# Optimization experiments

Measured on AMD Instinct MI355X. Metric: run time of the kernel, lower is better.

## Reference

```python
import jax, jax.numpy as jnp
import numpy as np

D = 1024   # dim_embedding
H = 16     # n_head
HD = D // H


def setup_inputs() -> dict:
    key = jax.random.key(0)
    ks = jax.random.split(key, 5)
    B, T = 2, 2048
    x = jax.random.normal(ks[0], (B, T, D), dtype=jnp.float32)
    e = jax.random.normal(ks[1], (B, T, D), dtype=jnp.float32)
    s = 0.02
    W_en = jax.random.normal(ks[2], (D, 2 * D), dtype=jnp.float32) * s   # c_attn_en (k,v from encoder)
    W_q = jax.random.normal(ks[3], (D, D), dtype=jnp.float32) * s        # c_attn (q from decoder)
    W_o = jax.random.normal(ks[4], (D, D), dtype=jnp.float32) * s        # c_proj
    return {"x": x, "e": e, "W_en": W_en, "W_q": W_q, "W_o": W_o}


def reference(x, e, W_en, W_q, W_o):
    B, T, C = e.shape
    kv = e @ W_en                       # [B,T,2C]
    k, v = jnp.split(kv, 2, axis=-1)    # [B,T,C] each
    q = x @ W_q                         # [B,T,C]
    # reshape to heads: [B,H,T,hd]
    q = q.reshape(B, T, H, HD).transpose(0, 2, 1, 3)
    k = k.reshape(B, T, H, HD).transpose(0, 2, 1, 3)
    v = v.reshape(B, T, H, HD).transpose(0, 2, 1, 3)
    att = jnp.einsum("bhqd,bhkd->bhqk", q, k) * (1.0 / jnp.sqrt(jnp.float32(HD)))
    att = jax.nn.softmax(att, axis=-1)  # dropout=0 (eval)
    y = jnp.einsum("bhqk,bhkd->bhqd", att, v)
    y = y.transpose(0, 2, 1, 3).reshape(B, T, C)
    return y @ W_o
```

## Files before the change

kernel.cpp:

```cpp
#include <hip/hip_runtime.h>

typedef unsigned short u16;
typedef unsigned int u32;
typedef __bf16 bf16x8 __attribute__((ext_vector_type(8)));
typedef float f32x4 __attribute__((ext_vector_type(4)));

#define D_EMB 1024
#define T_SEQ 2048
#define NH 16
#define HD 64

#define GLB(p) ((const __attribute__((address_space(1))) unsigned int*)(p))
#define LDSP(p) ((__attribute__((address_space(3))) unsigned int*)(p))

__device__ __forceinline__ u16 f2bf(float f) {
  union { float f; unsigned u; } c; c.f = f;
  unsigned u = c.u;
  unsigned r = (u + 0x7FFFu + ((u >> 16) & 1u)) >> 16;
  return (u16)r;
}
__device__ __forceinline__ u32 fbits(float f) {
  union { float f; unsigned u; } c; c.f = f; return c.u;
}

__global__ __launch_bounds__(256) void cvt_kernel(const float* __restrict__ in,
                                                  u16* __restrict__ out, int n4) {
  int i = blockIdx.x * 256 + threadIdx.x;
  if (i < n4) {
    float4 v = reinterpret_cast<const float4*>(in)[i];
    ushort4 o;
    o.x = f2bf(v.x); o.y = f2bf(v.y); o.z = f2bf(v.z); o.w = f2bf(v.w);
    reinterpret_cast<ushort4*>(out)[i] = o;
  }
}

__global__ __launch_bounds__(256) void tconv_kernel(const float* __restrict__ in,
                                                    u16* __restrict__ out, int K, int N) {
  __shared__ float tile[32][33];
  int n0 = blockIdx.x * 32, k0 = blockIdx.y * 32;
  int tx = threadIdx.x, ty = threadIdx.y;
#pragma unroll
  for (int s = 0; s < 4; s++)
    tile[ty + 8 * s][tx] = in[(size_t)(k0 + ty + 8 * s) * N + n0 + tx];
  __syncthreads();
#pragma unroll
  for (int s = 0; s < 4; s++)
    out[(size_t)(n0 + ty + 8 * s) * K + k0 + tx] = f2bf(tile[tx][ty + 8 * s]);
}

__global__ __launch_bounds__(256) void proj_kernel(
    const u16* __restrict__ xb, const u16* __restrict__ eb,
    const u16* __restrict__ Wqt, const u16* __restrict__ Went,
    u16* __restrict__ qw, u16* __restrict__ kw, u16* __restrict__ vTw) {
  __shared__ u16 Al[128 * 64];
  __shared__ u16 Bl[128 * 64];
  const int tid = threadIdx.x;
  const int nb = blockIdx.x, mb = blockIdx.y;
  const int wave = tid >> 6, lane = tid & 63;
  const int ln15 = lane & 15, quad = lane >> 4;
  const int wm = wave & 1, wn = wave >> 1;

  const u16* A = (nb < 8) ? xb : eb;
  const u16* Wt = (nb < 8) ? (Wqt + (size_t)nb * 128 * D_EMB)
                           : (Went + ((size_t)nb * 128 - D_EMB) * D_EMB);

  const int grow = wave * 8 + (lane >> 3);
  const int g = (lane & 7) ^ ((lane >> 3) & 7);
  const u16* gA = A + (size_t)(mb * 128 + grow) * D_EMB + g * 8;
  const u16* gB = Wt + (size_t)grow * D_EMB + g * 8;
  char* lA = (char*)Al + wave * 1024;
  char* lB = (char*)Bl + wave * 1024;

  f32x4 acc[4][4] = {};

  for (int kb = 0; kb < D_EMB; kb += 64) {
#pragma unroll
    for (int it = 0; it < 4; it++) {
      __builtin_amdgcn_global_load_lds(GLB(gA + (size_t)it * 32 * D_EMB + kb), LDSP(lA + it * 4096), 16, 0, 0);
      __builtin_amdgcn_global_load_lds(GLB(gB + (size_t)it * 32 * D_EMB + kb), LDSP(lB + it * 4096), 16, 0, 0);
    }
    __syncthreads();
#pragma unroll
    for (int ks = 0; ks < 2; ks++) {
      bf16x8 af[4], bfr[4];
#pragma unroll
      for (int mt = 0; mt < 4; mt++) {
        int r = wm * 64 + mt * 16 + ln15;
        af[mt] = *reinterpret_cast<const bf16x8*>(&Al[r * 64 + (((ks * 4 + quad) ^ (r & 7)) * 8)]);
      }
#pragma unroll
      for (int nt = 0; nt < 4; nt++) {
        int r = wn * 64 + nt * 16 + ln15;
        bfr[nt] = *reinterpret_cast<const bf16x8*>(&Bl[r * 64 + (((ks * 4 + quad) ^ (r & 7)) * 8)]);
      }
#pragma unroll
      for (int mt = 0; mt < 4; mt++)
#pragma unroll
        for (int nt = 0; nt < 4; nt++)
          acc[mt][nt] = __builtin_amdgcn_mfma_f32_16x16x32_bf16(af[mt], bfr[nt], acc[mt][nt], 0, 0, 0);
    }
    __syncthreads();
  }

  const float QSCL = 0.125f * 1.44269504f;
#pragma unroll
  for (int mt = 0; mt < 4; mt++) {
#pragma unroll
    for (int nt = 0; nt < 4; nt++) {
#pragma unroll
      for (int i = 0; i < 4; i++) {
        int rr = mb * 128 + wm * 64 + mt * 16 + quad * 4 + i;
        int c  = nb * 128 + wn * 64 + nt * 16 + ln15;
        float v = acc[mt][nt][i];
        int b = rr >> 11, t = rr & 2047;
        if (c < D_EMB) {
          int h = c >> 6, d = c & 63;
          qw[(((size_t)(b * NH + h)) * T_SEQ + t) * HD + d] = f2bf(v * QSCL);
        } else if (c < 2 * D_EMB) {
          int cc = c - D_EMB; int h = cc >> 6, d = cc & 63;
          kw[(((size_t)(b * NH + h)) * T_SEQ + t) * HD + d] = f2bf(v);
        } else {
          int cc = c - 2 * D_EMB; int h = cc >> 6, d = cc & 63;
          vTw[(((size_t)(b * NH + h)) * HD + d) * T_SEQ + t] = f2bf(v);
        }
      }
    }
  }
}

__global__ __launch_bounds__(256) void attn_kernel(
    const u16* __restrict__ q, const u16* __restrict__ k,
    const u16* __restrict__ vT, u16* __restrict__ y) {
  __shared__ u16 Kl[64][64];
  __shared__ u16 Vl[64][64];
  __shared__ u16 Pl[4][16][72];

  const int bh = blockIdx.y;
  const int qt = blockIdx.x;
  const int tid = threadIdx.x;
  const int wave = tid >> 6, lane = tid & 63;
  const int ln15 = lane & 15, quad = lane >> 4;
  const int b = bh >> 4, h = bh & 15;

  const int qrow = qt * 64 + wave * 16 + ln15;
  const u16* qbase = q + ((size_t)bh * T_SEQ + qrow) * HD;
  bf16x8 qf[2];
  qf[0] = *reinterpret_cast<const bf16x8*>(qbase + quad * 8);
  qf[1] = *reinterpret_cast<const bf16x8*>(qbase + 32 + quad * 8);

  f32x4 o[4] = {};
  float lp = 0.f;

  const int srow = (lane >> 3) & 7;
  const int sch  = lane & 7;
  const int gch  = sch ^ srow;
  const u16* kg0 = k  + ((size_t)bh * T_SEQ + wave * 16 + srow) * HD + gch * 8;
  const u16* kg1 = kg0 + 8 * HD;
  const u16* vg0 = vT + ((size_t)bh * HD + wave * 16 + srow) * T_SEQ + gch * 8;
  const u16* vg1 = vg0 + 8 * T_SEQ;
  char* klb = (char*)&Kl[0][0] + wave * 2048;
  char* vlb = (char*)&Vl[0][0] + wave * 2048;

  for (int kt0 = 0; kt0 < T_SEQ; kt0 += 64) {
    __builtin_amdgcn_global_load_lds(GLB(kg0 + (size_t)kt0 * HD), LDSP(klb),        16, 0, 0);
    __builtin_amdgcn_global_load_lds(GLB(kg1 + (size_t)kt0 * HD), LDSP(klb + 1024), 16, 0, 0);
    __builtin_amdgcn_global_load_lds(GLB(vg0 + kt0),              LDSP(vlb),        16, 0, 0);
    __builtin_amdgcn_global_load_lds(GLB(vg1 + kt0),              LDSP(vlb + 1024), 16, 0, 0);
    __syncthreads();

    f32x4 s[4] = {};
#pragma unroll
    for (int ks = 0; ks < 2; ks++)
#pragma unroll
      for (int nt = 0; nt < 4; nt++) {
        int r = nt * 16 + ln15;
        bf16x8 kf = *reinterpret_cast<const bf16x8*>(&Kl[r][(((ks * 4 + quad) ^ (r & 7)) * 8)]);
        s[nt] = __builtin_amdgcn_mfma_f32_16x16x32_bf16(kf, qf[ks], s[nt], 0, 0, 0);
      }

#pragma unroll
    for (int nt = 0; nt < 4; nt++) {
      float p0 = __builtin_amdgcn_exp2f(s[nt][0]);
      float p1 = __builtin_amdgcn_exp2f(s[nt][1]);
      float p2 = __builtin_amdgcn_exp2f(s[nt][2]);
      float p3 = __builtin_amdgcn_exp2f(s[nt][3]);
      lp += (p0 + p1) + (p2 + p3);
      u32 dw0 = __builtin_amdgcn_perm(fbits(p1), fbits(p0), 0x07060302u);
      u32 dw1 = __builtin_amdgcn_perm(fbits(p3), fbits(p2), 0x07060302u);
      *reinterpret_cast<uint2*>(&Pl[wave][ln15][nt * 16 + quad * 4]) = make_uint2(dw0, dw1);
    }
    asm volatile("s_waitcnt lgkmcnt(0)" ::: "memory");

#pragma unroll
    for (int ks = 0; ks < 2; ks++) {
      bf16x8 pf = *reinterpret_cast<const bf16x8*>(&Pl[wave][ln15][ks * 32 + quad * 8]);
#pragma unroll
      for (int nt = 0; nt < 4; nt++) {
        int r = nt * 16 + ln15;
        bf16x8 vf = *reinterpret_cast<const bf16x8*>(&Vl[r][(((ks * 4 + quad) ^ (r & 7)) * 8)]);
        o[nt] = __builtin_amdgcn_mfma_f32_16x16x32_bf16(vf, pf, o[nt], 0, 0, 0);
      }
    }
    __syncthreads();
  }

  lp += __shfl_xor(lp, 16, 64);
  lp += __shfl_xor(lp, 32, 64);
  const float inv = 1.0f / lp;

  const size_t ybase = ((size_t)b * T_SEQ + qrow) * D_EMB + h * 64;
#pragma unroll
  for (int nt = 0; nt < 4; nt++) {
    u16 b0 = f2bf(o[nt][0] * inv), b1 = f2bf(o[nt][1] * inv);
    u16 b2 = f2bf(o[nt][2] * inv), b3 = f2bf(o[nt][3] * inv);
    u32 dw0 = (u32)b0 | ((u32)b1 << 16);
    u32 dw1 = (u32)b2 | ((u32)b3 << 16);
    *reinterpret_cast<uint2*>(&y[ybase + nt * 16 + quad * 4]) = make_uint2(dw0, dw1);
  }
}

__global__ __launch_bounds__(256) void oproj_kernel(
    const u16* __restrict__ yw, const u16* __restrict__ Wot, float* __restrict__ out) {
  __shared__ u16 Al[128 * 64];
  __shared__ u16 Bl[128 * 64];
  const int tid = threadIdx.x;
  const int nb = blockIdx.x, mb = blockIdx.y;
  const int wave = tid >> 6, lane = tid & 63;
  const int ln15 = lane & 15, quad = lane >> 4;
  const int wm = wave & 1, wn = wave >> 1;

  const u16* Wt = Wot + (size_t)nb * 128 * D_EMB;
  const int grow = wave * 8 + (lane >> 3);
  const int g = (lane & 7) ^ ((lane >> 3) & 7);
  const u16* gA = yw + (size_t)(mb * 128 + grow) * D_EMB + g * 8;
  const u16* gB = Wt + (size_t)grow * D_EMB + g * 8;
  char* lA = (char*)Al + wave * 1024;
  char* lB = (char*)Bl + wave * 1024;

  f32x4 acc[4][4] = {};

  for (int kb = 0; kb < D_EMB; kb += 64) {
#pragma unroll
    for (int it = 0; it < 4; it++) {
      __builtin_amdgcn_global_load_lds(GLB(gA + (size_t)it * 32 * D_EMB + kb), LDSP(lA + it * 4096), 16, 0, 0);
      __builtin_amdgcn_global_load_lds(GLB(gB + (size_t)it * 32 * D_EMB + kb), LDSP(lB + it * 4096), 16, 0, 0);
    }
    __syncthreads();
#pragma unroll
    for (int ks = 0; ks < 2; ks++) {
      bf16x8 af[4], bfr[4];
#pragma unroll
      for (int mt = 0; mt < 4; mt++) {
        int r = wm * 64 + mt * 16 + ln15;
        af[mt] = *reinterpret_cast<const bf16x8*>(&Al[r * 64 + (((ks * 4 + quad) ^ (r & 7)) * 8)]);
      }
#pragma unroll
      for (int nt = 0; nt < 4; nt++) {
        int r = wn * 64 + nt * 16 + ln15;
        bfr[nt] = *reinterpret_cast<const bf16x8*>(&Bl[r * 64 + (((ks * 4 + quad) ^ (r & 7)) * 8)]);
      }
#pragma unroll
      for (int mt = 0; mt < 4; mt++)
#pragma unroll
        for (int nt = 0; nt < 4; nt++)
          acc[mt][nt] = __builtin_amdgcn_mfma_f32_16x16x32_bf16(af[mt], bfr[nt], acc[mt][nt], 0, 0, 0);
    }
    __syncthreads();
  }

#pragma unroll
  for (int mt = 0; mt < 4; mt++)
#pragma unroll
    for (int nt = 0; nt < 4; nt++)
#pragma unroll
      for (int i = 0; i < 4; i++) {
        int rr = mb * 128 + wm * 64 + mt * 16 + quad * 4 + i;
        int c  = nb * 128 + wn * 64 + nt * 16 + ln15;
        out[(size_t)rr * D_EMB + c] = acc[mt][nt][i];
      }
}

extern "C" void kernel_launch(void* const* d_in, const int* in_sizes, int n_in,
                              void* d_out, int out_size, void* d_ws, size_t ws_size,
                              hipStream_t stream) {
  const float* x    = (const float*)d_in[0];
  const float* e    = (const float*)d_in[1];
  const float* W_en = (const float*)d_in[2];
  const float* W_q  = (const float*)d_in[3];
  const float* W_o  = (const float*)d_in[4];
  float* out = (float*)d_out;

  char* w = (char*)d_ws;
  u16* xb   = (u16*)(w);
  u16* eb   = (u16*)(w + (8u  << 20));
  u16* Wqt  = (u16*)(w + (16u << 20));
  u16* Went = (u16*)(w + (18u << 20));
  u16* Wot  = (u16*)(w + (22u << 20));
  u16* qw   = (u16*)(w + (24u << 20));
  u16* kw   = (u16*)(w + (32u << 20));
  u16* vT   = (u16*)(w + (40u << 20));
  u16* yw   = (u16*)(w + (48u << 20));

  const int n4 = (2 * T_SEQ * D_EMB) / 4;
  cvt_kernel<<<(n4 + 255) / 256, 256, 0, stream>>>(x, xb, n4);
  cvt_kernel<<<(n4 + 255) / 256, 256, 0, stream>>>(e, eb, n4);
  tconv_kernel<<<dim3(D_EMB / 32, D_EMB / 32), dim3(32, 8), 0, stream>>>(W_q, Wqt, D_EMB, D_EMB);
  tconv_kernel<<<dim3(2 * D_EMB / 32, D_EMB / 32), dim3(32, 8), 0, stream>>>(W_en, Went, D_EMB, 2 * D_EMB);
  tconv_kernel<<<dim3(D_EMB / 32, D_EMB / 32), dim3(32, 8), 0, stream>>>(W_o, Wot, D_EMB, D_EMB);

  proj_kernel<<<dim3(24, 32), 256, 0, stream>>>(xb, eb, Wqt, Went, qw, kw, vT);
  attn_kernel<<<dim3(T_SEQ / 64, 32), 256, 0, stream>>>(qw, kw, vT, yw);
  oproj_kernel<<<dim3(8, 32), 256, 0, stream>>>(yw, Wot, out);
}
```

Before: 232.2 us.

## Fuse prep kernels and restructure attention with 32x32 MFMA and double-buffered K/V

The five fp32-to-bf16 convert and transpose launches are merged into one prep kernel, cutting launch overhead. The attention kernel now gives each wave 32 query rows (128 per block) and uses 32x32x16 MFMAs, which doubles K/V reuse per LDS load. K/V tiles are double-buffered so the next tile's global-to-LDS DMA overlaps the current tile's compute. The P staging buffer is also swizzled. In exchange the attention grid is halved to 512 blocks, and each thread holds more accumulator registers, which may lower occupancy.

```diff
diff --git a/kernel.cpp b/kernel.cpp
--- a/kernel.cpp
+++ b/kernel.cpp
@@ -4,6 +4,7 @@
 typedef unsigned int u32;
 typedef __bf16 bf16x8 __attribute__((ext_vector_type(8)));
 typedef float f32x4 __attribute__((ext_vector_type(4)));
+typedef float f32x16 __attribute__((ext_vector_type(16)));
 
 #define D_EMB 1024
 #define T_SEQ 2048
@@ -23,22 +24,30 @@
   union { float f; unsigned u; } c; c.f = f; return c.u;
 }
 
-__global__ __launch_bounds__(256) void cvt_kernel(const float* __restrict__ in,
-                                                  u16* __restrict__ out, int n4) {
-  int i = blockIdx.x * 256 + threadIdx.x;
-  if (i < n4) {
+__global__ __launch_bounds__(256) void prep_kernel(
+    const float* __restrict__ x, const float* __restrict__ e,
+    const float* __restrict__ W_q, const float* __restrict__ W_en, const float* __restrict__ W_o,
+    u16* __restrict__ xb, u16* __restrict__ eb,
+    u16* __restrict__ Wqt, u16* __restrict__ Went, u16* __restrict__ Wot) {
+  __shared__ float tile[32][33];
+  const int bid = blockIdx.x, tid = threadIdx.x;
+  if (bid < 8192) {
+    const float* in = (bid < 4096) ? x : e;
+    u16* out = (bid < 4096) ? xb : eb;
+    int i = (bid & 4095) * 256 + tid;
     float4 v = reinterpret_cast<const float4*>(in)[i];
     ushort4 o;
     o.x = f2bf(v.x); o.y = f2bf(v.y); o.z = f2bf(v.z); o.w = f2bf(v.w);
     reinterpret_cast<ushort4*>(out)[i] = o;
-  }
-}
-
-__global__ __launch_bounds__(256) void tconv_kernel(const float* __restrict__ in,
-                                                    u16* __restrict__ out, int K, int N) {
-  __shared__ float tile[32][33];
-  int n0 = blockIdx.x * 32, k0 = blockIdx.y * 32;
-  int tx = threadIdx.x, ty = threadIdx.y;
+    return;
+  }
+  const float* in; u16* out; int K, N, bx, by;
+  int rem = bid - 8192;
+  if (rem < 1024)      { in = W_q;  out = Wqt;  K = 1024; N = 1024; bx = rem & 31;          by = rem >> 5; }
+  else if (rem < 3072) { int r2 = rem - 1024; in = W_en; out = Went; K = 1024; N = 2048; bx = r2 & 63; by = r2 >> 6; }
+  else                 { int r3 = rem - 3072; in = W_o;  out = Wot;  K = 1024; N = 1024; bx = r3 & 31; by = r3 >> 5; }
+  int tx = tid & 31, ty = tid >> 5;
+  int n0 = bx * 32, k0 = by * 32;
 #pragma unroll
   for (int s = 0; s < 4; s++)
     tile[ty + 8 * s][tx] = in[(size_t)(k0 + ty + 8 * s) * N + n0 + tx];
@@ -131,92 +140,105 @@
 __global__ __launch_bounds__(256) void attn_kernel(
     const u16* __restrict__ q, const u16* __restrict__ k,
     const u16* __restrict__ vT, u16* __restrict__ y) {
-  __shared__ u16 Kl[64][64];
-  __shared__ u16 Vl[64][64];
-  __shared__ u16 Pl[4][16][72];
+  __shared__ u16 Kl[2][64][64];
+  __shared__ u16 Vl[2][64][64];
+  __shared__ u16 Pl[4][32][64];
 
   const int bh = blockIdx.y;
   const int qt = blockIdx.x;
   const int tid = threadIdx.x;
   const int wave = tid >> 6, lane = tid & 63;
-  const int ln15 = lane & 15, quad = lane >> 4;
+  const int q32 = lane & 31, hi = lane >> 5;
   const int b = bh >> 4, h = bh & 15;
 
-  const int qrow = qt * 64 + wave * 16 + ln15;
+  const int qrow = qt * 128 + wave * 32 + q32;
   const u16* qbase = q + ((size_t)bh * T_SEQ + qrow) * HD;
-  bf16x8 qf[2];
-  qf[0] = *reinterpret_cast<const bf16x8*>(qbase + quad * 8);
-  qf[1] = *reinterpret_cast<const bf16x8*>(qbase + 32 + quad * 8);
-
-  f32x4 o[4] = {};
+  bf16x8 qf[4];
+#pragma unroll
+  for (int s = 0; s < 4; s++)
+    qf[s] = *reinterpret_cast<const bf16x8*>(qbase + s * 16 + hi * 8);
+
+  f32x16 o2[2] = {};
   float lp = 0.f;
 
   const int srow = (lane >> 3) & 7;
-  const int sch  = lane & 7;
-  const int gch  = sch ^ srow;
+  const int gch  = (lane & 7) ^ srow;
   const u16* kg0 = k  + ((size_t)bh * T_SEQ + wave * 16 + srow) * HD + gch * 8;
-  const u16* kg1 = kg0 + 8 * HD;
   const u16* vg0 = vT + ((size_t)bh * HD + wave * 16 + srow) * T_SEQ + gch * 8;
-  const u16* vg1 = vg0 + 8 * T_SEQ;
-  char* klb = (char*)&Kl[0][0] + wave * 2048;
-  char* vlb = (char*)&Vl[0][0] + wave * 2048;
-
-  for (int kt0 = 0; kt0 < T_SEQ; kt0 += 64) {
-    __builtin_amdgcn_global_load_lds(GLB(kg0 + (size_t)kt0 * HD), LDSP(klb),        16, 0, 0);
-    __builtin_amdgcn_global_load_lds(GLB(kg1 + (size_t)kt0 * HD), LDSP(klb + 1024), 16, 0, 0);
-    __builtin_amdgcn_global_load_lds(GLB(vg0 + kt0),              LDSP(vlb),        16, 0, 0);
-    __builtin_amdgcn_global_load_lds(GLB(vg1 + kt0),              LDSP(vlb + 1024), 16, 0, 0);
-    __syncthreads();
-
-    f32x4 s[4] = {};
-#pragma unroll
-    for (int ks = 0; ks < 2; ks++)
-#pragma unroll
-      for (int nt = 0; nt < 4; nt++) {
-        int r = nt * 16 + ln15;
-        bf16x8 kf = *reinterpret_cast<const bf16x8*>(&Kl[r][(((ks * 4 + quad) ^ (r & 7)) * 8)]);
-        s[nt] = __builtin_amdgcn_mfma_f32_16x16x32_bf16(kf, qf[ks], s[nt], 0, 0, 0);
-      }
-
-#pragma unroll
-    for (int nt = 0; nt < 4; nt++) {
-      float p0 = __builtin_amdgcn_exp2f(s[nt][0]);
-      float p1 = __builtin_amdgcn_exp2f(s[nt][1]);
-      float p2 = __builtin_amdgcn_exp2f(s[nt][2]);
-      float p3 = __builtin_amdgcn_exp2f(s[nt][3]);
-      lp += (p0 + p1) + (p2 + p3);
-      u32 dw0 = __builtin_amdgcn_perm(fbits(p1), fbits(p0), 0x07060302u);
-      u32 dw1 = __builtin_amdgcn_perm(fbits(p3), fbits(p2), 0x07060302u);
-      *reinterpret_cast<uint2*>(&Pl[wave][ln15][nt * 16 + quad * 4]) = make_uint2(dw0, dw1);
-    }
+
+  auto issue_dma = [&](int t, int buf) {
+    char* klb = (char*)&Kl[buf][0][0] + wave * 2048;
+    char* vlb = (char*)&Vl[buf][0][0] + wave * 2048;
+    const u16* kp = kg0 + (size_t)t * 64 * HD;
+    const u16* vp = vg0 + t * 64;
+    __builtin_amdgcn_global_load_lds(GLB(kp),           LDSP(klb),        16, 0, 0);
+    __builtin_amdgcn_global_load_lds(GLB(kp + 8 * HD),  LDSP(klb + 1024), 16, 0, 0);
+    __builtin_amdgcn_global_load_lds(GLB(vp),           LDSP(vlb),        16, 0, 0);
+    __builtin_amdgcn_global_load_lds(GLB(vp + 8 * T_SEQ), LDSP(vlb + 1024), 16, 0, 0);
+  };
+
+  issue_dma(0, 0);
+
+  for (int t = 0; t < 32; t++) {
+    const int buf = t & 1;
+    __syncthreads();
+    if (t < 31) issue_dma(t + 1, buf ^ 1);
+
+    f32x16 s2[2] = {};
+#pragma unroll
+    for (int s = 0; s < 4; s++)
+#pragma unroll
+      for (int kt2 = 0; kt2 < 2; kt2++) {
+        int r = kt2 * 32 + q32;
+        bf16x8 kf = *reinterpret_cast<const bf16x8*>(
+            &Kl[buf][r][(((s * 2 + hi) ^ (r & 7)) * 8)]);
+        s2[kt2] = __builtin_amdgcn_mfma_f32_32x32x16_bf16(kf, qf[s], s2[kt2], 0, 0, 0);
+      }
+
+#pragma unroll
+    for (int kt2 = 0; kt2 < 2; kt2++)
+#pragma unroll
+      for (int g = 0; g < 4; g++) {
+        float p0 = __builtin_amdgcn_exp2f(s2[kt2][4 * g + 0]);
+        float p1 = __builtin_amdgcn_exp2f(s2[kt2][4 * g + 1]);
+        float p2 = __builtin_amdgcn_exp2f(s2[kt2][4 * g + 2]);
+        float p3 = __builtin_amdgcn_exp2f(s2[kt2][4 * g + 3]);
+        lp += (p0 + p1) + (p2 + p3);
+        u32 dw0 = __builtin_amdgcn_perm(fbits(p1), fbits(p0), 0x07060302u);
+        u32 dw1 = __builtin_amdgcn_perm(fbits(p3), fbits(p2), 0x07060302u);
+        int phys = (kt2 * 4 + g) ^ (q32 & 7);
+        *reinterpret_cast<uint2*>(&Pl[wave][q32][phys * 8 + 4 * hi]) = make_uint2(dw0, dw1);
+      }
     asm volatile("s_waitcnt lgkmcnt(0)" ::: "memory");
 
 #pragma unroll
-    for (int ks = 0; ks < 2; ks++) {
-      bf16x8 pf = *reinterpret_cast<const bf16x8*>(&Pl[wave][ln15][ks * 32 + quad * 8]);
-#pragma unroll
-      for (int nt = 0; nt < 4; nt++) {
-        int r = nt * 16 + ln15;
-        bf16x8 vf = *reinterpret_cast<const bf16x8*>(&Vl[r][(((ks * 4 + quad) ^ (r & 7)) * 8)]);
-        o[nt] = __builtin_amdgcn_mfma_f32_16x16x32_bf16(vf, pf, o[nt], 0, 0, 0);
-      }
-    }
-    __syncthreads();
-  }
-
-  lp += __shfl_xor(lp, 16, 64);
+    for (int s = 0; s < 4; s++) {
+      bf16x8 pf = *reinterpret_cast<const bf16x8*>(
+          &Pl[wave][q32][(((s * 2 + hi) ^ (q32 & 7)) * 8)]);
+#pragma unroll
+      for (int dt = 0; dt < 2; dt++) {
+        int r = dt * 32 + q32;
+        bf16x8 vf = *reinterpret_cast<const bf16x8*>(
+            &Vl[buf][r][(((s * 2 + hi) ^ (r & 7)) * 8)]);
+        o2[dt] = __builtin_amdgcn_mfma_f32_32x32x16_bf16(vf, pf, o2[dt], 0, 0, 0);
+      }
+    }
+  }
+
   lp += __shfl_xor(lp, 32, 64);
   const float inv = 1.0f / lp;
 
   const size_t ybase = ((size_t)b * T_SEQ + qrow) * D_EMB + h * 64;
 #pragma unroll
-  for (int nt = 0; nt < 4; nt++) {
-    u16 b0 = f2bf(o[nt][0] * inv), b1 = f2bf(o[nt][1] * inv);
-    u16 b2 = f2bf(o[nt][2] * inv), b3 = f2bf(o[nt][3] * inv);
-    u32 dw0 = (u32)b0 | ((u32)b1 << 16);
-    u32 dw1 = (u32)b2 | ((u32)b3 << 16);
-    *reinterpret_cast<uint2*>(&y[ybase + nt * 16 + quad * 4]) = make_uint2(dw0, dw1);
-  }
+  for (int dt = 0; dt < 2; dt++)
+#pragma unroll
+    for (int g = 0; g < 4; g++) {
+      u16 b0 = f2bf(o2[dt][4 * g + 0] * inv), b1 = f2bf(o2[dt][4 * g + 1] * inv);
+      u16 b2 = f2bf(o2[dt][4 * g + 2] * inv), b3 = f2bf(o2[dt][4 * g + 3] * inv);
+      u32 dw0 = (u32)b0 | ((u32)b1 << 16);
+      u32 dw1 = (u32)b2 | ((u32)b3 << 16);
+      *reinterpret_cast<uint2*>(&y[ybase + dt * 32 + 8 * g + 4 * hi]) = make_uint2(dw0, dw1);
+    }
 }
 
 __global__ __launch_bounds__(256) void oproj_kernel(
@@ -301,14 +323,8 @@
   u16* vT   = (u16*)(w + (40u << 20));
   u16* yw   = (u16*)(w + (48u << 20));
 
-  const int n4 = (2 * T_SEQ * D_EMB) / 4;
-  cvt_kernel<<<(n4 + 255) / 256, 256, 0, stream>>>(x, xb, n4);
-  cvt_kernel<<<(n4 + 255) / 256, 256, 0, stream>>>(e, eb, n4);
-  tconv_kernel<<<dim3(D_EMB / 32, D_EMB / 32), dim3(32, 8), 0, stream>>>(W_q, Wqt, D_EMB, D_EMB);
-  tconv_kernel<<<dim3(2 * D_EMB / 32, D_EMB / 32), dim3(32, 8), 0, stream>>>(W_en, Went, D_EMB, 2 * D_EMB);
-  tconv_kernel<<<dim3(D_EMB / 32, D_EMB / 32), dim3(32, 8), 0, stream>>>(W_o, Wot, D_EMB, D_EMB);
-
+  prep_kernel<<<12288, 256, 0, stream>>>(x, e, W_q, W_en, W_o, xb, eb, Wqt, Went, Wot);
   proj_kernel<<<dim3(24, 32), 256, 0, stream>>>(xb, eb, Wqt, Went, qw, kw, vT);
-  attn_kernel<<<dim3(T_SEQ / 64, 32), 256, 0, stream>>>(qw, kw, vT, yw);
+  attn_kernel<<<dim3(T_SEQ / 128, 32), 256, 0, stream>>>(qw, kw, vT, yw);
   oproj_kernel<<<dim3(8, 32), 256, 0, stream>>>(yw, Wot, out);
 }
```

New measurement: 225.3 us. -3.0%, faster.
